# Optimization experiments

Measured on AMD Instinct MI355X. Metric: run time of the kernel, lower is better.

Reference implementation:

```python
import jax, jax.numpy as jnp
import numpy as np

B, C, H, W = 8, 256, 128, 128


def setup_inputs() -> dict:
    key = jax.random.key(0)
    k1, k2, k3, k4, k5 = jax.random.split(key, 5)
    x = jax.random.normal(k1, (B, C, H, W), dtype=jnp.float32)
    # 1x1 conv weights stored as (out_channels, in_channels); bias (out_channels,)
    w1 = jax.random.normal(k2, (C, C), dtype=jnp.float32) * (1.0 / np.sqrt(C))
    b1 = jax.random.normal(k3, (C,), dtype=jnp.float32) * 0.01
    w2 = jax.random.normal(k4, (C, C), dtype=jnp.float32) * (1.0 / np.sqrt(C))
    b2 = jax.random.normal(k5, (C,), dtype=jnp.float32) * 0.01
    return {"x": x, "w1": w1, "b1": b1, "w2": w2, "b2": b2}


def reference(x, w1, b1, w2, b2):
    b, c, h, w = x.shape
    xf = x.reshape(b, c, h * w)                      # (B, C, N)
    # 1x1 convs == per-pixel linear maps over channels
    q = jnp.einsum('oc,bcn->bon', w1, xf) + b1[None, :, None]   # (B, C, N)
    k = jnp.einsum('oc,bcn->bon', w2, xf) + b2[None, :, None]   # (B, C, N)
    # channel-attention Gram matrix: (B, C, N) @ (B, N, C) -> (B, C, C)
    attention = jnp.einsum('bcn,bdn->bcd', q, k)
    attention = jax.nn.softmax(attention, axis=-1)
    # (B, C, C) @ (B, C, N) -> (B, C, N), v = x itself (unprojected)
    attention_v = jnp.einsum('bcd,bdn->bcn', attention, xf).reshape(b, c, h, w)
    return x + attention_v
```

## Files before the change

kernel.cpp:

```cpp
#include <hip/hip_runtime.h>
#include <hip/hip_bf16.h>

#define B_    8
#define C_    256
#define NPIX  16384
#define BK    64
#define KC4   16
#define KCH4  (NPIX / KC4)
#define NSTEP4 (KCH4 / BK)

typedef __attribute__((ext_vector_type(8))) short bf16x8;
typedef __attribute__((ext_vector_type(4))) float f32x4;
typedef unsigned int uint_;

__device__ __forceinline__ unsigned short f2bf(float x) {
  unsigned int u = __builtin_bit_cast(unsigned int, x);
  u = (u + 0x7fffu + ((u >> 16) & 1u)) >> 16;
  return (unsigned short)u;
}

__global__ __launch_bounds__(512, 2) void k_gram(const float* __restrict__ x,
                                                 float* __restrict__ gpart,
                                                 float* __restrict__ spart) {
  const int bid  = blockIdx.x;
  const int half = bid >> 7;
  const int b    = (bid >> 4) & 7;
  const int kc   = bid & 15;
  const float* X = x + (size_t)b * C_ * NPIX + kc * KCH4;

  __shared__ __align__(16) unsigned short Hi[2][256 * 64];
  __shared__ __align__(16) unsigned short Lo[2][256 * 64];

  const int tid  = threadIdx.x;
  const int lane = tid & 63;
  const int w    = tid >> 6;
  const int wr   = w >> 2;
  const int wc   = w & 3;

  const int srow = tid >> 4;
  const int scol = (tid & 15) * 4;
  const float* sp = X + (size_t)srow * NPIX + scol;

  float rs[8] = {};
  float4 g[8];

#define GLOAD(ks)                                                             \
  _Pragma("unroll")                                                           \
  for (int j = 0; j < 8; ++j)                                                 \
    g[j] = *reinterpret_cast<const float4*>(sp + (size_t)j * 32 * NPIX + (ks) * BK);

#define STAGE(buf)                                                            \
  _Pragma("unroll")                                                           \
  for (int j = 0; j < 8; ++j) {                                               \
    const float4 v = g[j];                                                    \
    rs[j] += (v.x + v.y) + (v.z + v.w);                                       \
    const uint_ u0 = __builtin_bit_cast(uint_, v.x);                          \
    const uint_ u1 = __builtin_bit_cast(uint_, v.y);                          \
    const uint_ u2 = __builtin_bit_cast(uint_, v.z);                          \
    const uint_ u3 = __builtin_bit_cast(uint_, v.w);                          \
    uint2 hi, lo;                                                             \
    hi.x = (u0 >> 16) | (u1 & 0xffff0000u);                                   \
    hi.y = (u2 >> 16) | (u3 & 0xffff0000u);                                   \
    const float h0 = __builtin_bit_cast(float, u0 & 0xffff0000u);             \
    const float h1 = __builtin_bit_cast(float, u1 & 0xffff0000u);             \
    const float h2 = __builtin_bit_cast(float, u2 & 0xffff0000u);             \
    const float h3 = __builtin_bit_cast(float, u3 & 0xffff0000u);             \
    const uint_ l0 = __builtin_bit_cast(uint_, v.x - h0);                     \
    const uint_ l1 = __builtin_bit_cast(uint_, v.y - h1);                     \
    const uint_ l2 = __builtin_bit_cast(uint_, v.z - h2);                     \
    const uint_ l3 = __builtin_bit_cast(uint_, v.w - h3);                     \
    lo.x = (l0 >> 16) | (l1 & 0xffff0000u);                                   \
    lo.y = (l2 >> 16) | (l3 & 0xffff0000u);                                   \
    const int row = j * 32 + srow;                                            \
    const int idx = (row * 64 + scol) ^ ((row & 7) << 3);                     \
    *reinterpret_cast<uint2*>(&Hi[buf][idx]) = hi;                            \
    *reinterpret_cast<uint2*>(&Lo[buf][idx]) = lo;                            \
  }

  GLOAD(0)
  STAGE(0)
  __syncthreads();

  f32x4 acc[4][4] = {};

  for (int ks = 0; ks < NSTEP4; ++ks) {
    const int cur = ks & 1;
    if (ks + 1 < NSTEP4) GLOAD(ks + 1)
    __builtin_amdgcn_s_setprio(1);
#pragma unroll
    for (int kk = 0; kk < 2; ++kk) {
      const int kb = kk * 32 + (lane >> 4) * 8;
      bf16x8 ahi[4], bhi[4], blo[4];
#pragma unroll
      for (int m = 0; m < 4; ++m) {
        const int row = half * 128 + wr * 64 + m * 16 + (lane & 15);
        ahi[m] = *reinterpret_cast<const bf16x8*>(&Hi[cur][(row * 64 + kb) ^ ((row & 7) << 3)]);
      }
#pragma unroll
      for (int n = 0; n < 4; ++n) {
        const int row = wc * 64 + n * 16 + (lane & 15);
        bhi[n] = *reinterpret_cast<const bf16x8*>(&Hi[cur][(row * 64 + kb) ^ ((row & 7) << 3)]);
      }
#pragma unroll
      for (int m = 0; m < 4; ++m)
#pragma unroll
        for (int n = 0; n < 4; ++n)
          acc[m][n] = __builtin_amdgcn_mfma_f32_16x16x32_bf16(ahi[m], bhi[n], acc[m][n], 0, 0, 0);
#pragma unroll
      for (int n = 0; n < 4; ++n) {
        const int row = wc * 64 + n * 16 + (lane & 15);
        blo[n] = *reinterpret_cast<const bf16x8*>(&Lo[cur][(row * 64 + kb) ^ ((row & 7) << 3)]);
      }
#pragma unroll
      for (int m = 0; m < 4; ++m)
#pragma unroll
        for (int n = 0; n < 4; ++n)
          acc[m][n] = __builtin_amdgcn_mfma_f32_16x16x32_bf16(ahi[m], blo[n], acc[m][n], 0, 0, 0);
#pragma unroll
      for (int m = 0; m < 4; ++m) {
        const int row = half * 128 + wr * 64 + m * 16 + (lane & 15);
        bf16x8 alo = *reinterpret_cast<const bf16x8*>(&Lo[cur][(row * 64 + kb) ^ ((row & 7) << 3)]);
#pragma unroll
        for (int n = 0; n < 4; ++n)
          acc[m][n] = __builtin_amdgcn_mfma_f32_16x16x32_bf16(alo, bhi[n], acc[m][n], 0, 0, 0);
      }
    }
    __builtin_amdgcn_s_setprio(0);
    if (ks + 1 < NSTEP4) STAGE(cur ^ 1)
    __syncthreads();
  }
#undef GLOAD
#undef STAGE

#pragma unroll
  for (int j = 0; j < 8; ++j) {
#pragma unroll
    for (int off = 1; off < 16; off <<= 1) rs[j] += __shfl_xor(rs[j], off, 64);
  }
  if (half == 0 && (tid & 15) == 0) {
#pragma unroll
    for (int j = 0; j < 8; ++j)
      spart[((size_t)b * KC4 + kc) * 256 + j * 32 + srow] = rs[j];
  }

  float* gp = gpart + (size_t)bid * (128 * 256);
#pragma unroll
  for (int m = 0; m < 4; ++m) {
    const int row0 = wr * 64 + m * 16 + ((lane >> 4) << 2);
#pragma unroll
    for (int n = 0; n < 4; ++n) {
      const int col = wc * 64 + n * 16 + (lane & 15);
#pragma unroll
      for (int j = 0; j < 4; ++j)
        gp[(size_t)(row0 + j) * 256 + col] = acc[m][n][j];
    }
  }
}

__global__ __launch_bounds__(256) void k_reduce(const float* __restrict__ gpart,
                                                float* __restrict__ G) {
  const int t  = blockIdx.x * 256 + threadIdx.x;
  const int b  = t >> 14;
  const int i  = (t >> 6) & 255;
  const int j4 = (t & 63) * 4;
  const int hb = (i >> 7) * 128 + b * 16;
  const int il = i & 127;
  float4 s = make_float4(0.f, 0.f, 0.f, 0.f);
#pragma unroll
  for (int kc = 0; kc < KC4; ++kc) {
    const float4 v = *reinterpret_cast<const float4*>(
        &gpart[(size_t)(hb + kc) * (128 * 256) + (size_t)il * 256 + j4]);
    s.x += v.x; s.y += v.y; s.z += v.z; s.w += v.w;
  }
  *reinterpret_cast<float4*>(&G[((size_t)b * 256 + i) * 256 + j4]) = s;
}

__global__ __launch_bounds__(256) void k_transpose(const float* __restrict__ in,
                                                   float* __restrict__ outp) {
  __shared__ float t[32][33];
  const int bx = blockIdx.x & 7, by = blockIdx.x >> 3;
  const int tx = threadIdx.x & 31, ty = threadIdx.x >> 5;
#pragma unroll
  for (int i = 0; i < 32; i += 8)
    t[ty + i][tx] = in[(size_t)(by * 32 + ty + i) * 256 + bx * 32 + tx];
  __syncthreads();
#pragma unroll
  for (int i = 0; i < 32; i += 8)
    outp[(size_t)(bx * 32 + ty + i) * 256 + by * 32 + tx] = t[tx][ty + i];
}

__global__ __launch_bounds__(256) void k_u(const float* __restrict__ w1,
                                           const float* __restrict__ w2,
                                           const float* __restrict__ spart,
                                           float* __restrict__ u1,
                                           float* __restrict__ u2) {
  const int b = blockIdx.x;
  const int tid = threadIdx.x;
  __shared__ float sl[256];
  float sv = 0.f;
#pragma unroll
  for (int kc = 0; kc < KC4; ++kc) sv += spart[((size_t)b * KC4 + kc) * 256 + tid];
  sl[tid] = sv;
  __syncthreads();
  float a1 = 0.f, a2 = 0.f;
#pragma unroll 4
  for (int c = 0; c < 256; ++c) {
    a1 += w1[(size_t)tid * 256 + c] * sl[c];
    a2 += w2[(size_t)tid * 256 + c] * sl[c];
  }
  u1[b * 256 + tid] = a1;
  u2[b * 256 + tid] = a2;
}

__global__ __launch_bounds__(256) void k_smallmm(const float* __restrict__ A, long asb,
                                                 const float* __restrict__ Bm, long bsb,
                                                 float* __restrict__ Cm, long csb) {
  const int b  = blockIdx.y;
  const int i0 = blockIdx.x * 8;
  const float* Ab = A  + (size_t)asb * b;
  const float* Bb = Bm + (size_t)bsb * b;
  float*       Cb = Cm + (size_t)csb * b;
  const int tid = threadIdx.x;
  __shared__ float arows[8][256];
#pragma unroll
  for (int rr = 0; rr < 8; ++rr) arows[rr][tid] = Ab[(size_t)(i0 + rr) * 256 + tid];
  __syncthreads();
  float acc[8] = {};
#pragma unroll 4
  for (int k = 0; k < 256; ++k) {
    const float bv = Bb[(size_t)k * 256 + tid];
#pragma unroll
    for (int rr = 0; rr < 8; ++rr) acc[rr] += arows[rr][k] * bv;
  }
#pragma unroll
  for (int rr = 0; rr < 8; ++rr) Cb[(size_t)(i0 + rr) * 256 + tid] = acc[rr];
}

__global__ __launch_bounds__(256) void k_softmax(const float* __restrict__ L,
                                                 const float* __restrict__ b1,
                                                 const float* __restrict__ b2,
                                                 const float* __restrict__ u1,
                                                 const float* __restrict__ u2,
                                                 unsigned short* __restrict__ Abf) {
  const int b = blockIdx.y, i = blockIdx.x, j = threadIdx.x;
  const size_t base = ((size_t)b * 256 + i) * 256;
  const float v = L[base + j] + u1[b * 256 + i] * b2[j] +
                  b1[i] * (u2[b * 256 + j] + 16384.f * b2[j]);
  const int lane = j & 63, wv = j >> 6;
  __shared__ float redm[4], reds[4];
  float m = v;
#pragma unroll
  for (int off = 32; off; off >>= 1) m = fmaxf(m, __shfl_xor(m, off, 64));
  if (lane == 0) redm[wv] = m;
  __syncthreads();
  m = fmaxf(fmaxf(redm[0], redm[1]), fmaxf(redm[2], redm[3]));
  const float e = __expf(v - m);
  float sm = e;
#pragma unroll
  for (int off = 32; off; off >>= 1) sm += __shfl_xor(sm, off, 64);
  if (lane == 0) reds[wv] = sm;
  __syncthreads();
  sm = (reds[0] + reds[1]) + (reds[2] + reds[3]);
  Abf[base + j] = f2bf(e / sm);
}

__global__ __launch_bounds__(512, 4) void k_av(const unsigned short* __restrict__ Abf,
                                               const float* __restrict__ x,
                                               float* __restrict__ out) {
  const int bx = blockIdx.x;
  const int b  = bx & 7;
  const int n0 = (bx >> 3) * 64;
  const unsigned short* Ab = Abf + (size_t)b * 65536;
  const float* Xb = x   + (size_t)b * C_ * NPIX;
  float*       Ob = out + (size_t)b * C_ * NPIX;

  __shared__ __align__(16) unsigned short Xt[64 * 256];

  const int tid = threadIdx.x;
  const int lane = tid & 63, w = tid >> 6;
  const int wc2 = w >> 1, wn = w & 1;

#pragma unroll
  for (int h = 0; h < 2; ++h) {
    const int d  = (tid >> 4) * 4 + h * 128;
    const int nn = (tid & 15) * 4;
    const float* xs = Xb + (size_t)d * NPIX + n0 + nn;
    float4 r0 = *reinterpret_cast<const float4*>(xs);
    float4 r1 = *reinterpret_cast<const float4*>(xs + NPIX);
    float4 r2 = *reinterpret_cast<const float4*>(xs + 2 * NPIX);
    float4 r3 = *reinterpret_cast<const float4*>(xs + 3 * NPIX);
    ushort4 c0 = make_ushort4(f2bf(r0.x), f2bf(r1.x), f2bf(r2.x), f2bf(r3.x));
    ushort4 c1 = make_ushort4(f2bf(r0.y), f2bf(r1.y), f2bf(r2.y), f2bf(r3.y));
    ushort4 c2 = make_ushort4(f2bf(r0.z), f2bf(r1.z), f2bf(r2.z), f2bf(r3.z));
    ushort4 c3 = make_ushort4(f2bf(r0.w), f2bf(r1.w), f2bf(r2.w), f2bf(r3.w));
    const int i0 = ((nn + 0) * 256 + d) ^ (((nn + 0) & 7) << 3);
    const int i1 = ((nn + 1) * 256 + d) ^ (((nn + 1) & 7) << 3);
    const int i2 = ((nn + 2) * 256 + d) ^ (((nn + 2) & 7) << 3);
    const int i3 = ((nn + 3) * 256 + d) ^ (((nn + 3) & 7) << 3);
    *reinterpret_cast<ushort4*>(&Xt[i0]) = c0;
    *reinterpret_cast<ushort4*>(&Xt[i1]) = c1;
    *reinterpret_cast<ushort4*>(&Xt[i2]) = c2;
    *reinterpret_cast<ushort4*>(&Xt[i3]) = c3;
  }
  __syncthreads();

  f32x4 acc[4][2] = {};
  bf16x8 af0[4], af1[4];
  bf16x8 bq0[2], bq1[2];

#define LOADFR(kk, af, bq)                                                    \
  {                                                                           \
    const int kb = (kk) * 32 + (lane >> 4) * 8;                               \
    _Pragma("unroll")                                                         \
    for (int m = 0; m < 4; ++m) {                                             \
      const int c = wc2 * 64 + m * 16 + (lane & 15);                          \
      uint4 v = *reinterpret_cast<const uint4*>(Ab + (size_t)c * 256 + kb);   \
      af[m] = __builtin_bit_cast(bf16x8, v);                                  \
    }                                                                         \
    _Pragma("unroll")                                                         \
    for (int n = 0; n < 2; ++n) {                                             \
      const int nn2 = wn * 32 + n * 16 + (lane & 15);                         \
      bq[n] = *reinterpret_cast<const bf16x8*>(&Xt[(nn2 * 256 + kb) ^ ((nn2 & 7) << 3)]); \
    }                                                                         \
  }
#define MFMA8(af, bq)                                                         \
  _Pragma("unroll")                                                           \
  for (int m = 0; m < 4; ++m)                                                 \
    _Pragma("unroll")                                                         \
    for (int n = 0; n < 2; ++n)                                               \
      acc[m][n] = __builtin_amdgcn_mfma_f32_16x16x32_bf16(af[m], bq[n], acc[m][n], 0, 0, 0);

  LOADFR(0, af0, bq0)
#pragma unroll
  for (int kk = 0; kk < 8; kk += 2) {
    if (kk + 1 < 8) LOADFR(kk + 1, af1, bq1)
    MFMA8(af0, bq0)
    if (kk + 2 < 8) LOADFR(kk + 2, af0, bq0)
    MFMA8(af1, bq1)
  }
#undef LOADFR
#undef MFMA8

#pragma unroll
  for (int m = 0; m < 4; ++m) {
    const int row0 = wc2 * 64 + m * 16 + ((lane >> 4) << 2);
#pragma unroll
    for (int n = 0; n < 2; ++n) {
      const int col = n0 + wn * 32 + n * 16 + (lane & 15);
#pragma unroll
      for (int j = 0; j < 4; ++j) {
        const size_t a = (size_t)(row0 + j) * NPIX + col;
        Ob[a] = Xb[a] + acc[m][n][j];
      }
    }
  }
}

extern "C" void kernel_launch(void* const* d_in, const int* in_sizes, int n_in,
                              void* d_out, int out_size, void* d_ws, size_t ws_size,
                              hipStream_t stream) {
  const float* x  = (const float*)d_in[0];
  const float* w1 = (const float*)d_in[1];
  const float* b1 = (const float*)d_in[2];
  const float* w2 = (const float*)d_in[3];
  const float* b2 = (const float*)d_in[4];
  float* out = (float*)d_out;
  char* ws = (char*)d_ws;

  float* gpart = out;

  constexpr size_t G_OFF     = 0;
  constexpr size_t T1_OFF    = G_OFF   + (size_t)B_ * C_ * C_ * 4;
  constexpr size_t L_OFF     = T1_OFF  + (size_t)B_ * C_ * C_ * 4;
  constexpr size_t W2T_OFF   = L_OFF   + (size_t)B_ * C_ * C_ * 4;
  constexpr size_t SPART_OFF = W2T_OFF + (size_t)C_ * C_ * 4;
  constexpr size_t U1_OFF    = SPART_OFF + (size_t)B_ * KC4 * C_ * 4;
  constexpr size_t U2_OFF    = U1_OFF  + (size_t)B_ * C_ * 4;
  constexpr size_t ABF_OFF   = U2_OFF  + (size_t)B_ * C_ * 4;

  float* G     = (float*)(ws + G_OFF);
  float* T1    = (float*)(ws + T1_OFF);
  float* L     = (float*)(ws + L_OFF);
  float* w2t   = (float*)(ws + W2T_OFF);
  float* spart = (float*)(ws + SPART_OFF);
  float* u1    = (float*)(ws + U1_OFF);
  float* u2    = (float*)(ws + U2_OFF);
  unsigned short* Abf = (unsigned short*)(ws + ABF_OFF);

  k_transpose<<<64, 256, 0, stream>>>(w2, w2t);
  k_gram     <<<256, 512, 0, stream>>>(x, gpart, spart);
  k_reduce   <<<512, 256, 0, stream>>>(gpart, G);
  k_u        <<<B_, 256, 0, stream>>>(w1, w2, spart, u1, u2);
  k_smallmm  <<<dim3(32, B_), 256, 0, stream>>>(w1, 0, G, C_ * C_, T1, C_ * C_);
  k_smallmm  <<<dim3(32, B_), 256, 0, stream>>>(T1, C_ * C_, w2t, 0, L, C_ * C_);
  k_softmax  <<<dim3(C_, B_), 256, 0, stream>>>(L, b1, b2, u1, u2, Abf);
  k_av       <<<dim3(NPIX / 64 * B_), 512, 0, stream>>>(Abf, x, out);
}
```

Before: 235.1 us.

## Make k_av persistent over four pixel tiles with double-buffered LDS prefetch

After: 354.8 us. 1.51x slower.

```diff
diff --git a/kernel.cpp b/kernel.cpp
--- a/kernel.cpp
+++ b/kernel.cpp
@@ -17,6 +17,9 @@
   unsigned int u = __builtin_bit_cast(unsigned int, x);
   u = (u + 0x7fffu + ((u >> 16) & 1u)) >> 16;
   return (unsigned short)u;
+}
+__device__ __forceinline__ float fcomp(const float4& v, int i) {
+  switch (i) { case 0: return v.x; case 1: return v.y; case 2: return v.z; default: return v.w; }
 }
 
 __global__ __launch_bounds__(512, 2) void k_gram(const float* __restrict__ x,
@@ -267,93 +270,107 @@
 __global__ __launch_bounds__(512, 4) void k_av(const unsigned short* __restrict__ Abf,
                                                const float* __restrict__ x,
                                                float* __restrict__ out) {
-  const int bx = blockIdx.x;
-  const int b  = bx & 7;
-  const int n0 = (bx >> 3) * 64;
+  const int bid = blockIdx.x;
+  const int b = bid & 7;
+  const int nbase = (bid >> 3) * 256;
   const unsigned short* Ab = Abf + (size_t)b * 65536;
-  const float* Xb = x   + (size_t)b * C_ * NPIX;
-  float*       Ob = out + (size_t)b * C_ * NPIX;
-
-  __shared__ __align__(16) unsigned short Xt[64 * 256];
+  const float* Xb = x + (size_t)b * C_ * NPIX;
+  float* Ob = out + (size_t)b * C_ * NPIX;
+
+  __shared__ __align__(16) unsigned short Xt[2][64 * 256];
 
   const int tid = threadIdx.x;
   const int lane = tid & 63, w = tid >> 6;
   const int wc2 = w >> 1, wn = w & 1;
-
-#pragma unroll
-  for (int h = 0; h < 2; ++h) {
-    const int d  = (tid >> 4) * 4 + h * 128;
-    const int nn = (tid & 15) * 4;
-    const float* xs = Xb + (size_t)d * NPIX + n0 + nn;
-    float4 r0 = *reinterpret_cast<const float4*>(xs);
-    float4 r1 = *reinterpret_cast<const float4*>(xs + NPIX);
-    float4 r2 = *reinterpret_cast<const float4*>(xs + 2 * NPIX);
-    float4 r3 = *reinterpret_cast<const float4*>(xs + 3 * NPIX);
-    ushort4 c0 = make_ushort4(f2bf(r0.x), f2bf(r1.x), f2bf(r2.x), f2bf(r3.x));
-    ushort4 c1 = make_ushort4(f2bf(r0.y), f2bf(r1.y), f2bf(r2.y), f2bf(r3.y));
-    ushort4 c2 = make_ushort4(f2bf(r0.z), f2bf(r1.z), f2bf(r2.z), f2bf(r3.z));
-    ushort4 c3 = make_ushort4(f2bf(r0.w), f2bf(r1.w), f2bf(r2.w), f2bf(r3.w));
-    const int i0 = ((nn + 0) * 256 + d) ^ (((nn + 0) & 7) << 3);
-    const int i1 = ((nn + 1) * 256 + d) ^ (((nn + 1) & 7) << 3);
-    const int i2 = ((nn + 2) * 256 + d) ^ (((nn + 2) & 7) << 3);
-    const int i3 = ((nn + 3) * 256 + d) ^ (((nn + 3) & 7) << 3);
-    *reinterpret_cast<ushort4*>(&Xt[i0]) = c0;
-    *reinterpret_cast<ushort4*>(&Xt[i1]) = c1;
-    *reinterpret_cast<ushort4*>(&Xt[i2]) = c2;
-    *reinterpret_cast<ushort4*>(&Xt[i3]) = c3;
-  }
-  __syncthreads();
-
-  f32x4 acc[4][2] = {};
-  bf16x8 af0[4], af1[4];
-  bf16x8 bq0[2], bq1[2];
-
-#define LOADFR(kk, af, bq)                                                    \
-  {                                                                           \
-    const int kb = (kk) * 32 + (lane >> 4) * 8;                               \
-    _Pragma("unroll")                                                         \
-    for (int m = 0; m < 4; ++m) {                                             \
-      const int c = wc2 * 64 + m * 16 + (lane & 15);                          \
-      uint4 v = *reinterpret_cast<const uint4*>(Ab + (size_t)c * 256 + kb);   \
-      af[m] = __builtin_bit_cast(bf16x8, v);                                  \
-    }                                                                         \
-    _Pragma("unroll")                                                         \
-    for (int n = 0; n < 2; ++n) {                                             \
-      const int nn2 = wn * 32 + n * 16 + (lane & 15);                         \
-      bq[n] = *reinterpret_cast<const bf16x8*>(&Xt[(nn2 * 256 + kb) ^ ((nn2 & 7) << 3)]); \
-    }                                                                         \
-  }
-#define MFMA8(af, bq)                                                         \
+  const int dgrp = tid >> 4, d0 = dgrp * 8, nnb = (tid & 15) * 4;
+  const float* xsb = Xb + (size_t)d0 * NPIX + nbase + nnb;
+
+  float4 gld[8];
+
+#define GLD(t)                                                                \
+  _Pragma("unroll")                                                           \
+  for (int r = 0; r < 8; ++r)                                                 \
+    gld[r] = *reinterpret_cast<const float4*>(xsb + (size_t)r * NPIX + (t) * 64);
+
+#define CONV(buf)                                                             \
+  _Pragma("unroll")                                                           \
+  for (int i = 0; i < 4; ++i) {                                               \
+    uint4 v;                                                                  \
+    v.x = (uint_)f2bf(fcomp(gld[0], i)) | ((uint_)f2bf(fcomp(gld[1], i)) << 16); \
+    v.y = (uint_)f2bf(fcomp(gld[2], i)) | ((uint_)f2bf(fcomp(gld[3], i)) << 16); \
+    v.z = (uint_)f2bf(fcomp(gld[4], i)) | ((uint_)f2bf(fcomp(gld[5], i)) << 16); \
+    v.w = (uint_)f2bf(fcomp(gld[6], i)) | ((uint_)f2bf(fcomp(gld[7], i)) << 16); \
+    const int row = nnb + i;                                                  \
+    const int idx = (row * 256 + d0) ^ (((row ^ (row >> 2)) & 7) << 3);       \
+    *reinterpret_cast<uint4*>(&Xt[buf][idx]) = v;                             \
+  }
+
+#define LOADA(kk, af)                                                         \
+  _Pragma("unroll")                                                           \
+  for (int m = 0; m < 4; ++m)                                                 \
+    af[m] = *reinterpret_cast<const bf16x8*>(                                 \
+        Ab + (size_t)(wc2 * 64 + m * 16 + (lane & 15)) * 256 + (kk) * 32 + kboff);
+
+#define LOADB(kk, buf)                                                        \
+  _Pragma("unroll")                                                           \
+  for (int n = 0; n < 2; ++n) {                                               \
+    const int nn2 = wn * 32 + n * 16 + (lane & 15);                           \
+    bq[n] = *reinterpret_cast<const bf16x8*>(                                 \
+        &Xt[buf][(nn2 * 256 + (kk) * 32 + kboff) ^ (((nn2 ^ (nn2 >> 2)) & 7) << 3)]); \
+  }
+
+#define MFMA8(af)                                                             \
   _Pragma("unroll")                                                           \
   for (int m = 0; m < 4; ++m)                                                 \
     _Pragma("unroll")                                                         \
     for (int n = 0; n < 2; ++n)                                               \
       acc[m][n] = __builtin_amdgcn_mfma_f32_16x16x32_bf16(af[m], bq[n], acc[m][n], 0, 0, 0);
 
-  LOADFR(0, af0, bq0)
-#pragma unroll
-  for (int kk = 0; kk < 8; kk += 2) {
-    if (kk + 1 < 8) LOADFR(kk + 1, af1, bq1)
-    MFMA8(af0, bq0)
-    if (kk + 2 < 8) LOADFR(kk + 2, af0, bq0)
-    MFMA8(af1, bq1)
-  }
-#undef LOADFR
+  const int kboff = (lane >> 4) * 8;
+
+  GLD(0)
+
+#pragma unroll
+  for (int t = 0; t < 4; ++t) {
+    const int buf = t & 1;
+    CONV(buf)
+    __syncthreads();
+
+    bf16x8 afA[4], afB[4], bq[2];
+    LOADA(0, afA)
+    if (t < 3) GLD(t + 1)
+
+    f32x4 acc[4][2] = {};
+    __builtin_amdgcn_s_setprio(1);
+#pragma unroll
+    for (int kk = 0; kk < 8; ++kk) {
+      LOADB(kk, buf)
+      if (kk < 7) {
+        if (kk & 1) { LOADA(kk + 1, afA) } else { LOADA(kk + 1, afB) }
+      }
+      if (kk & 1) { MFMA8(afB) } else { MFMA8(afA) }
+    }
+    __builtin_amdgcn_s_setprio(0);
+
+#pragma unroll
+    for (int m = 0; m < 4; ++m) {
+      const int row0 = wc2 * 64 + m * 16 + ((lane >> 4) << 2);
+#pragma unroll
+      for (int n = 0; n < 2; ++n) {
+        const int col = nbase + t * 64 + wn * 32 + n * 16 + (lane & 15);
+#pragma unroll
+        for (int j = 0; j < 4; ++j) {
+          const size_t a = (size_t)(row0 + j) * NPIX + col;
+          Ob[a] = Xb[a] + acc[m][n][j];
+        }
+      }
+    }
+  }
+#undef GLD
+#undef CONV
+#undef LOADA
+#undef LOADB
 #undef MFMA8
-
-#pragma unroll
-  for (int m = 0; m < 4; ++m) {
-    const int row0 = wc2 * 64 + m * 16 + ((lane >> 4) << 2);
-#pragma unroll
-    for (int n = 0; n < 2; ++n) {
-      const int col = n0 + wn * 32 + n * 16 + (lane & 15);
-#pragma unroll
-      for (int j = 0; j < 4; ++j) {
-        const size_t a = (size_t)(row0 + j) * NPIX + col;
-        Ob[a] = Xb[a] + acc[m][n][j];
-      }
-    }
-  }
 }
 
 extern "C" void kernel_launch(void* const* d_in, const int* in_sizes, int n_in,
@@ -394,5 +411,5 @@
   k_smallmm  <<<dim3(32, B_), 256, 0, stream>>>(w1, 0, G, C_ * C_, T1, C_ * C_);
   k_smallmm  <<<dim3(32, B_), 256, 0, stream>>>(T1, C_ * C_, w2t, 0, L, C_ * C_);
   k_softmax  <<<dim3(C_, B_), 256, 0, stream>>>(L, b1, b2, u1, u2, Abf);
-  k_av       <<<dim3(NPIX / 64 * B_), 512, 0, stream>>>(Abf, x, out);
-}
+  k_av       <<<512, 512, 0, stream>>>(Abf, x, out);
+}
```
